# Kernel tuning notes

Hardware: AMD Instinct MI355X
Metric: run time of the kernel (lower is better)

Reference implementation:

```python
import jax, jax.numpy as jnp
import numpy as np

Q, N, D = 4096, 50000, 64

def setup_inputs() -> dict:
    key = jax.random.key(0)
    k1, k2, k3, k4 = jax.random.split(key, 4)
    features = jax.random.normal(k1, (Q, D), dtype=jnp.float32)
    # bw_transform is a (lower-triangular cholesky) bandwidth transform; a small
    # random matrix is fine for a numerical reference. Scale down so exp(-d2/2)
    # does not underflow everywhere.
    bw_transform = jax.random.normal(k2, (D, D), dtype=jnp.float32) * 0.05
    dataset = jax.random.normal(k3, (N, D), dtype=jnp.float32)
    norm = jax.random.uniform(k4, (1,), dtype=jnp.float32)
    return {"features": features, "bw_transform": bw_transform, "dataset": dataset, "norm": norm}

def reference(features, bw_transform, dataset, norm):
    # features: [Q, D], bw_transform: [D, D], dataset: [N, D] (already transformed), norm: [1]
    f = features @ bw_transform  # [Q, D]
    # pairwise squared distances via expansion: ||f||^2 + ||x||^2 - 2 f.x
    f2 = jnp.sum(f * f, axis=1)            # [Q]
    x2 = jnp.sum(dataset * dataset, axis=1)  # [N]
    d2 = f2[:, None] + x2[None, :] - 2.0 * (f @ dataset.T)  # [Q, N]
    kern = jnp.exp(-0.5 * d2) * norm[0]    # [Q, N]
    estimate = jnp.mean(kern, axis=1)       # [Q]
    return estimate
```

## Files before the change

kernel.cpp:

```cpp
#include <hip/hip_runtime.h>


#define QCNT 4096
#define NCNT 50000
#define DDIM 64

#define SPLITS 64
#define NPB 832
#define NROWS (SPLITS * NPB)
#define NUNITS 26
#define QTILES (QCNT / 256)
#define SPLIT_HALVES (NPB * DDIM)

#define FSPLITS 32
#define FNPB 1563
#define FNITERS 25
#define BN 64

typedef _Float16 half8_t __attribute__((ext_vector_type(8)));
typedef float float4_t __attribute__((ext_vector_type(4)));

#define K2F 1.44269504088896340f
#define KC2 -0.72134752044448169f

#define PREP_F_BLOCKS (QCNT / 4)
#define PREP_X_BLOCKS (NROWS * 8 / 256)

__global__ void prep_fused(const float* __restrict__ features,
                           const float* __restrict__ bw,
                           const float* __restrict__ dataset,
                           _Float16* __restrict__ fh,
                           float* __restrict__ cf2,
                           _Float16* __restrict__ xhp,
                           float* __restrict__ ecxg) {
    if (blockIdx.x < PREP_F_BLOCKS) {
        const int lane = threadIdx.x & 63;
        const int q = blockIdx.x * 4 + (threadIdx.x >> 6);
        const float* frow = features + q * DDIM;
        float acc = 0.f;
#pragma unroll
        for (int k = 0; k < DDIM; ++k)
            acc = fmaf(frow[k], bw[k * DDIM + lane], acc);
        fh[(size_t)q * DDIM + lane] = (_Float16)(K2F * acc);
        float s = acc * acc;
#pragma unroll
        for (int m = 1; m < 64; m <<= 1) s += __shfl_xor(s, m, 64);
        if (lane == 0) cf2[q] = KC2 * s;
    } else {
        const int t = (blockIdx.x - PREP_F_BLOCKS) * 256 + threadIdx.x;
        const int row = t >> 3;
        const int c = t & 7;
        if (row >= NROWS) return;
        float4_t v0 = {0.f, 0.f, 0.f, 0.f}, v1 = {0.f, 0.f, 0.f, 0.f};
        if (row < NCNT) {
            const float4_t* src = (const float4_t*)(dataset + (size_t)row * DDIM + c * 8);
            v0 = src[0]; v1 = src[1];
        }
        float s = v0[0]*v0[0] + v0[1]*v0[1] + v0[2]*v0[2] + v0[3]*v0[3]
                + v1[0]*v1[0] + v1[1]*v1[1] + v1[2]*v1[2] + v1[3]*v1[3];
        s += __shfl_xor(s, 1, 64);
        s += __shfl_xor(s, 2, 64);
        s += __shfl_xor(s, 4, 64);
        if (c == 0) ecxg[row] = (row < NCNT) ? __builtin_amdgcn_exp2f(KC2 * s) : 0.f;
        half8_t h;
        h[0] = (_Float16)v0[0]; h[1] = (_Float16)v0[1];
        h[2] = (_Float16)v0[2]; h[3] = (_Float16)v0[3];
        h[4] = (_Float16)v1[0]; h[5] = (_Float16)v1[1];
        h[6] = (_Float16)v1[2]; h[7] = (_Float16)v1[3];
        const int split = row / NPB;
        const int nr = row - split * NPB;
        const int it = nr >> 6;
        const int brow = nr & 63;
        const int nt = brow >> 4;
        const int l15 = brow & 15;
        const int f = c >> 2;
        const int lh = c & 3;
        const int lane = lh * 16 + l15;
        const size_t base = ((((size_t)split * 13 + it) * 4 + nt) * 2 + f) * 512;
        *(half8_t*)(xhp + base + lane * 8) = h;
    }
}

__global__ __launch_bounds__(256, 4)
void kde_main_fast(const _Float16* __restrict__ fh,
                   const float* __restrict__ ecxg,
                   const _Float16* __restrict__ xhp,
                   float* __restrict__ partial) {
    __shared__ float lecx[NPB];

    const int tid = threadIdx.x;
    const int lane = tid & 63;
    const int w = tid >> 6;
    const int l15 = lane & 15;
    const int lh = lane >> 4;

    const int bid = blockIdx.x;
    const int xcd = bid & 7;
    const int j = bid >> 3;
    const int split = xcd * 8 + (j & 7);
    const int qtile = j >> 3;

    const int qbase = qtile * 256 + w * 64;

    half8_t a[4][2];
#pragma unroll
    for (int qt = 0; qt < 4; ++qt)
#pragma unroll
        for (int kt = 0; kt < 2; ++kt)
            a[qt][kt] = *(const half8_t*)(fh + (size_t)(qbase + qt * 16 + l15) * DDIM
                                             + kt * 32 + lh * 8);

    {
        const float* es = ecxg + (size_t)split * NPB;
        for (int i = tid; i < NPB; i += 256) lecx[i] = es[i];
    }
    __syncthreads();

    {
        const int skew = w + ((bid >> 3) & 3);
#pragma unroll 1
        for (int i = 0; i < skew; ++i) __builtin_amdgcn_s_sleep(2);
    }

    const _Float16* bs = xhp + (size_t)split * SPLIT_HALVES + (size_t)lane * 8;

    float sum[4][4];
#pragma unroll
    for (int qt = 0; qt < 4; ++qt)
#pragma unroll
        for (int r = 0; r < 4; ++r) sum[qt][r] = 0.f;

    const float4_t zc = {0.f, 0.f, 0.f, 0.f};

#define LOADU(P, u_)                                                          \
    {                                                                         \
        const _Float16* p_ = bs + (size_t)(u_) * 2048;                        \
        P[0][0] = *(const half8_t*)(p_);                                      \
        P[0][1] = *(const half8_t*)(p_ + 512);                                \
        P[1][0] = *(const half8_t*)(p_ + 1024);                               \
        P[1][1] = *(const half8_t*)(p_ + 1536);                               \
    }

#define COMPU(P, u_)                                                          \
    {                                                                         \
        _Pragma("unroll")                                                     \
        for (int s_ = 0; s_ < 2; ++s_) {                                      \
            const float e_ = lecx[(u_) * 32 + s_ * 16 + l15];                 \
            float4_t t0, t1, t2, t3;                                          \
            t0 = __builtin_amdgcn_mfma_f32_16x16x32_f16(a[0][0], P[s_][0], zc, 0, 0, 0); \
            t1 = __builtin_amdgcn_mfma_f32_16x16x32_f16(a[1][0], P[s_][0], zc, 0, 0, 0); \
            t2 = __builtin_amdgcn_mfma_f32_16x16x32_f16(a[2][0], P[s_][0], zc, 0, 0, 0); \
            t3 = __builtin_amdgcn_mfma_f32_16x16x32_f16(a[3][0], P[s_][0], zc, 0, 0, 0); \
            t0 = __builtin_amdgcn_mfma_f32_16x16x32_f16(a[0][1], P[s_][1], t0, 0, 0, 0); \
            t1 = __builtin_amdgcn_mfma_f32_16x16x32_f16(a[1][1], P[s_][1], t1, 0, 0, 0); \
            t2 = __builtin_amdgcn_mfma_f32_16x16x32_f16(a[2][1], P[s_][1], t2, 0, 0, 0); \
            t3 = __builtin_amdgcn_mfma_f32_16x16x32_f16(a[3][1], P[s_][1], t3, 0, 0, 0); \
            _Pragma("unroll")                                                 \
            for (int r = 0; r < 4; ++r) {                                     \
                sum[0][r] = fmaf(__builtin_amdgcn_exp2f(t0[r]), e_, sum[0][r]); \
                sum[1][r] = fmaf(__builtin_amdgcn_exp2f(t1[r]), e_, sum[1][r]); \
                sum[2][r] = fmaf(__builtin_amdgcn_exp2f(t2[r]), e_, sum[2][r]); \
                sum[3][r] = fmaf(__builtin_amdgcn_exp2f(t3[r]), e_, sum[3][r]); \
            }                                                                 \
        }                                                                     \
    }

    half8_t bA[2][2], bB[2][2];

    LOADU(bA, 0);
#pragma unroll 1
    for (int u = 0; u < NUNITS; u += 2) {
        LOADU(bB, u + 1);
        COMPU(bA, u);
        if (u + 2 < NUNITS) LOADU(bA, u + 2);
        COMPU(bB, u + 1);
    }

#pragma unroll
    for (int qt = 0; qt < 4; ++qt)
#pragma unroll
        for (int r = 0; r < 4; ++r) {
            float s = sum[qt][r];
            s += __shfl_xor(s, 1, 64);
            s += __shfl_xor(s, 2, 64);
            s += __shfl_xor(s, 4, 64);
            s += __shfl_xor(s, 8, 64);
            sum[qt][r] = s;
        }
    if (l15 == 0) {
        float* dst = partial + (size_t)split * QCNT + qbase;
#pragma unroll
        for (int qt = 0; qt < 4; ++qt)
#pragma unroll
            for (int r = 0; r < 4; ++r)
                dst[qt * 16 + lh * 4 + r] = sum[qt][r];
    }
#undef LOADU
#undef COMPU
}

__global__ void prep_f_kernel(const float* __restrict__ features,
                              const float* __restrict__ bw,
                              _Float16* __restrict__ fh,
                              float* __restrict__ cf2) {
    const int lane = threadIdx.x & 63;
    const int q = blockIdx.x * (blockDim.x >> 6) + (threadIdx.x >> 6);
    if (q >= QCNT) return;
    const float* frow = features + q * DDIM;
    float acc = 0.f;
#pragma unroll
    for (int k = 0; k < DDIM; ++k)
        acc = fmaf(frow[k], bw[k * DDIM + lane], acc);
    fh[(size_t)q * DDIM + lane] = (_Float16)(K2F * acc);
    float s = acc * acc;
#pragma unroll
    for (int m = 1; m < 64; m <<= 1) s += __shfl_xor(s, m, 64);
    if (lane == 0) cf2[q] = KC2 * s;
}

__global__ void prep_x2_kernel(const float* __restrict__ dataset,
                               float* __restrict__ cx2) {
    const int n = blockIdx.x * blockDim.x + threadIdx.x;
    if (n >= NCNT) return;
    const float4* row = (const float4*)(dataset + (size_t)n * DDIM);
    float s = 0.f;
#pragma unroll
    for (int jq = 0; jq < DDIM / 4; ++jq) {
        float4 v = row[jq];
        s += v.x * v.x + v.y * v.y + v.z * v.z + v.w * v.w;
    }
    cx2[n] = KC2 * s;
}

__global__ __launch_bounds__(256, 2)
void kde_main_fb(const _Float16* __restrict__ fh,
                 const float* __restrict__ cx2,
                 const float* __restrict__ dataset,
                 float* __restrict__ partial) {
    __shared__ __align__(16) _Float16 xt[BN * DDIM];
    const int tid = threadIdx.x;
    const int lane = tid & 63;
    const int w = tid >> 6;
    const int l15 = lane & 15;
    const int lh = lane >> 4;
    const int qbase = blockIdx.x * 256 + w * 64;
    const int nstart = blockIdx.y * FNPB;
    const int nlimit = min(nstart + FNPB, NCNT);

    half8_t a[4][2];
#pragma unroll
    for (int qt = 0; qt < 4; ++qt)
#pragma unroll
        for (int kt = 0; kt < 2; ++kt)
            a[qt][kt] = *(const half8_t*)(fh + (size_t)(qbase + qt * 16 + l15) * DDIM
                                             + kt * 32 + lh * 8);
    float sum[4][4];
#pragma unroll
    for (int qt = 0; qt < 4; ++qt)
#pragma unroll
        for (int r = 0; r < 4; ++r) sum[qt][r] = 0.f;

    const int sn = tid >> 2;
    const int sk = tid & 3;
    const int c0 = (sk * 2) ^ (sn & 7);
    const int c1 = (sk * 2 + 1) ^ (sn & 7);

    for (int it = 0; it < FNITERS; ++it) {
        const int nb = nstart + it * BN;
        __syncthreads();
        {
            const int ng = nb + sn;
            float4_t v0 = {0.f,0.f,0.f,0.f}, v1 = {0.f,0.f,0.f,0.f};
            float4_t v2 = {0.f,0.f,0.f,0.f}, v3 = {0.f,0.f,0.f,0.f};
            if (ng < nlimit) {
                const float4_t* src = (const float4_t*)(dataset + (size_t)ng * DDIM + sk * 16);
                v0 = src[0]; v1 = src[1]; v2 = src[2]; v3 = src[3];
            }
            half8_t h0, h1;
            h0[0]=(_Float16)v0[0]; h0[1]=(_Float16)v0[1]; h0[2]=(_Float16)v0[2]; h0[3]=(_Float16)v0[3];
            h0[4]=(_Float16)v1[0]; h0[5]=(_Float16)v1[1]; h0[6]=(_Float16)v1[2]; h0[7]=(_Float16)v1[3];
            h1[0]=(_Float16)v2[0]; h1[1]=(_Float16)v2[1]; h1[2]=(_Float16)v2[2]; h1[3]=(_Float16)v2[3];
            h1[4]=(_Float16)v3[0]; h1[5]=(_Float16)v3[1]; h1[6]=(_Float16)v3[2]; h1[7]=(_Float16)v3[3];
            *(half8_t*)(xt + sn * DDIM + c0 * 8) = h0;
            *(half8_t*)(xt + sn * DDIM + c1 * 8) = h1;
        }
        __syncthreads();
#pragma unroll
        for (int nt = 0; nt < 4; ++nt) {
            const int ng = nb + nt * 16 + l15;
            const float c2 = (ng < nlimit) ? cx2[ng] : -1.0e30f;
            const int brow = nt * 16 + l15;
            const half8_t b0 = *(const half8_t*)(xt + brow * DDIM + ((lh ^ (brow & 7)) * 8));
            const half8_t b1 = *(const half8_t*)(xt + brow * DDIM + (((4 + lh) ^ (brow & 7)) * 8));
#pragma unroll
            for (int qt = 0; qt < 4; ++qt) {
                float4_t c = {c2, c2, c2, c2};
                float4_t acc = __builtin_amdgcn_mfma_f32_16x16x32_f16(a[qt][0], b0, c, 0, 0, 0);
                acc = __builtin_amdgcn_mfma_f32_16x16x32_f16(a[qt][1], b1, acc, 0, 0, 0);
#pragma unroll
                for (int r = 0; r < 4; ++r)
                    sum[qt][r] += __builtin_amdgcn_exp2f(acc[r]);
            }
        }
    }
#pragma unroll
    for (int qt = 0; qt < 4; ++qt)
#pragma unroll
        for (int r = 0; r < 4; ++r) {
            float s = sum[qt][r];
            s += __shfl_xor(s, 1, 64);
            s += __shfl_xor(s, 2, 64);
            s += __shfl_xor(s, 4, 64);
            s += __shfl_xor(s, 8, 64);
            sum[qt][r] = s;
        }
    if (l15 == 0) {
        float* dst = partial + (size_t)blockIdx.y * QCNT + qbase;
#pragma unroll
        for (int qt = 0; qt < 4; ++qt)
#pragma unroll
            for (int r = 0; r < 4; ++r)
                dst[qt * 16 + lh * 4 + r] = sum[qt][r];
    }
}

__global__ void reduce_kernel(const float* __restrict__ partial,
                              const float* __restrict__ cf2,
                              const float* __restrict__ norm,
                              float* __restrict__ out, int splits) {
    const int q = blockIdx.x * blockDim.x + threadIdx.x;
    if (q >= QCNT) return;
    float s = 0.f;
    for (int sp = 0; sp < splits; ++sp) s += partial[(size_t)sp * QCNT + q];
    out[q] = s * __builtin_amdgcn_exp2f(cf2[q]) * norm[0] * (1.0f / (float)NCNT);
}

extern "C" void kernel_launch(void* const* d_in, const int* in_sizes, int n_in,
                              void* d_out, int out_size, void* d_ws, size_t ws_size,
                              hipStream_t stream) {
    const float* features = (const float*)d_in[0];
    const float* bw       = (const float*)d_in[1];
    const float* dataset  = (const float*)d_in[2];
    const float* norm     = (const float*)d_in[3];
    float* out = (float*)d_out;
    float* ws = (float*)d_ws;

    const size_t NEED = (size_t)(1703936 + 131072 + 4096 + 53248 + 262144) * 4;

    if (ws_size >= NEED) {
        _Float16* xhp = (_Float16*)ws;
        _Float16* fh  = (_Float16*)(ws + 1703936);
        float* cf2     = ws + 1703936 + 131072;
        float* ecxg    = cf2 + 4096;
        float* partial = ecxg + 53248;

        prep_fused<<<PREP_F_BLOCKS + PREP_X_BLOCKS, 256, 0, stream>>>(
            features, bw, dataset, fh, cf2, xhp, ecxg);
        kde_main_fast<<<QTILES * SPLITS, 256, 0, stream>>>(fh, ecxg, xhp, partial);
        reduce_kernel<<<QCNT / 256, 256, 0, stream>>>(partial, cf2, norm, out, SPLITS);
    } else {
        _Float16* fh = (_Float16*)ws;
        float* cf2     = ws + 131072;
        float* cx2     = ws + 131072 + 4096;
        float* partial = ws + 131072 + 4096 + 50176;

        prep_f_kernel<<<QCNT / 4, 256, 0, stream>>>(features, bw, fh, cf2);
        prep_x2_kernel<<<(NCNT + 255) / 256, 256, 0, stream>>>(dataset, cx2);
        dim3 grid(QCNT / 256, FSPLITS);
        kde_main_fb<<<grid, 256, 0, stream>>>(fh, cx2, dataset, partial);
        reduce_kernel<<<QCNT / 256, 256, 0, stream>>>(partial, cf2, norm, out, FSPLITS);
    }
}
```

Measured before the change: 66.48 us.

## Triple-buffer dataset loads, raise MFMA priority, and parallelize split reduction

The main loop moves from double to triple buffering of the per-unit fp16 dataset fragments, so loads are issued two units ahead of their MFMA use. s_setprio brackets each MFMA burst so that wave gets issue priority while the matrix ops are in flight. The reduce kernel now gives each query four threads, each summing a quarter of the splits and combining via shuffles, which adds parallelism to a short tail kernel. Costs are extra registers for the third buffer, which may lower occupancy, and a reduction that assumes the split count divides by four.

```diff
diff --git a/kernel.cpp b/kernel.cpp
--- a/kernel.cpp
+++ b/kernel.cpp
@@ -147,6 +147,7 @@
         for (int s_ = 0; s_ < 2; ++s_) {                                      \
             const float e_ = lecx[(u_) * 32 + s_ * 16 + l15];                 \
             float4_t t0, t1, t2, t3;                                          \
+            __builtin_amdgcn_s_setprio(1);                                    \
             t0 = __builtin_amdgcn_mfma_f32_16x16x32_f16(a[0][0], P[s_][0], zc, 0, 0, 0); \
             t1 = __builtin_amdgcn_mfma_f32_16x16x32_f16(a[1][0], P[s_][0], zc, 0, 0, 0); \
             t2 = __builtin_amdgcn_mfma_f32_16x16x32_f16(a[2][0], P[s_][0], zc, 0, 0, 0); \
@@ -155,6 +156,7 @@
             t1 = __builtin_amdgcn_mfma_f32_16x16x32_f16(a[1][1], P[s_][1], t1, 0, 0, 0); \
             t2 = __builtin_amdgcn_mfma_f32_16x16x32_f16(a[2][1], P[s_][1], t2, 0, 0, 0); \
             t3 = __builtin_amdgcn_mfma_f32_16x16x32_f16(a[3][1], P[s_][1], t3, 0, 0, 0); \
+            __builtin_amdgcn_s_setprio(0);                                    \
             _Pragma("unroll")                                                 \
             for (int r = 0; r < 4; ++r) {                                     \
                 sum[0][r] = fmaf(__builtin_amdgcn_exp2f(t0[r]), e_, sum[0][r]); \
@@ -165,16 +167,18 @@
         }                                                                     \
     }
 
-    half8_t bA[2][2], bB[2][2];
+    half8_t bA[2][2], bB[2][2], bC[2][2];
 
     LOADU(bA, 0);
+    LOADU(bB, 1);
 #pragma unroll 1
-    for (int u = 0; u < NUNITS; u += 2) {
-        LOADU(bB, u + 1);
-        COMPU(bA, u);
-        if (u + 2 < NUNITS) LOADU(bA, u + 2);
-        COMPU(bB, u + 1);
-    }
+    for (int u = 0; u < 24; u += 3) {
+        LOADU(bC, u + 2); COMPU(bA, u);
+        LOADU(bA, u + 3); COMPU(bB, u + 1);
+        LOADU(bB, u + 4); COMPU(bC, u + 2);
+    }
+    COMPU(bA, 24);
+    COMPU(bB, 25);
 
 #pragma unroll
     for (int qt = 0; qt < 4; ++qt)
@@ -328,11 +332,18 @@
                               const float* __restrict__ cf2,
                               const float* __restrict__ norm,
                               float* __restrict__ out, int splits) {
-    const int q = blockIdx.x * blockDim.x + threadIdx.x;
+    const int t = blockIdx.x * blockDim.x + threadIdx.x;
+    const int q = t >> 2;
+    const int sub = t & 3;
     if (q >= QCNT) return;
+    const int per = splits >> 2;
     float s = 0.f;
-    for (int sp = 0; sp < splits; ++sp) s += partial[(size_t)sp * QCNT + q];
-    out[q] = s * __builtin_amdgcn_exp2f(cf2[q]) * norm[0] * (1.0f / (float)NCNT);
+    for (int sp = sub * per; sp < (sub + 1) * per; ++sp)
+        s += partial[(size_t)sp * QCNT + q];
+    s += __shfl_xor(s, 1, 64);
+    s += __shfl_xor(s, 2, 64);
+    if (sub == 0)
+        out[q] = s * __builtin_amdgcn_exp2f(cf2[q]) * norm[0] * (1.0f / (float)NCNT);
 }
 
 extern "C" void kernel_launch(void* const* d_in, const int* in_sizes, int n_in,
@@ -357,7 +368,7 @@
         prep_fused<<<PREP_F_BLOCKS + PREP_X_BLOCKS, 256, 0, stream>>>(
             features, bw, dataset, fh, cf2, xhp, ecxg);
         kde_main_fast<<<QTILES * SPLITS, 256, 0, stream>>>(fh, ecxg, xhp, partial);
-        reduce_kernel<<<QCNT / 256, 256, 0, stream>>>(partial, cf2, norm, out, SPLITS);
+        reduce_kernel<<<(QCNT * 4) / 256, 256, 0, stream>>>(partial, cf2, norm, out, SPLITS);
     } else {
         _Float16* fh = (_Float16*)ws;
         float* cf2     = ws + 131072;
@@ -368,6 +379,6 @@
         prep_x2_kernel<<<(NCNT + 255) / 256, 256, 0, stream>>>(dataset, cx2);
         dim3 grid(QCNT / 256, FSPLITS);
         kde_main_fb<<<grid, 256, 0, stream>>>(fh, cx2, dataset, partial);
-        reduce_kernel<<<QCNT / 256, 256, 0, stream>>>(partial, cf2, norm, out, FSPLITS);
-    }
-}
+        reduce_kernel<<<(QCNT * 4) / 256, 256, 0, stream>>>(partial, cf2, norm, out, FSPLITS);
+    }
+}
```

Result: slower. 94.44 us (+42.1%).
